# Kernel optimization log

Hardware: AMD Instinct MI355X
Metric: run time of the kernel (lower is better)

The kernel has to match this reference:

```python
import jax, jax.numpy as jnp
import numpy as np


def _gcn_conv(h, src, dst, W, b, n):
    # PyG GCNConv: x @ W, then symmetric-normalized aggregation with self-loops
    deg = jax.ops.segment_sum(jnp.ones(src.shape[0], h.dtype), dst, num_segments=n)
    dinv = jax.lax.rsqrt(jnp.maximum(deg, 1.0))  # deg >= 1 because self-loops are included
    norm = dinv[src] * dinv[dst]                 # [E]
    m = (h @ W)[src] * norm[:, None]             # gather + scale
    return jax.ops.segment_sum(m, dst, num_segments=n) + b


def setup_inputs() -> dict:
    key = jax.random.key(0)
    N, E, F, H, L, V = 50000, 800000, 128, 256, 64, 128
    ks = jax.random.split(key, 16)
    s = lambda fan_in: 1.0 / np.sqrt(fan_in)
    return {
        "x": jax.random.randint(ks[0], (N,), 0, V),
        "edge_index": jax.random.randint(ks[1], (2, E), 0, N),
        "eps": jax.random.normal(ks[2], (N, L), jnp.float32),
        "emb": jax.random.normal(ks[3], (V, F), jnp.float32),
        "W1": jax.random.normal(ks[4], (F, H), jnp.float32) * s(F),
        "b1": jnp.zeros((H,), jnp.float32),
        "W2": jax.random.normal(ks[5], (H, H), jnp.float32) * s(H),
        "b2": jnp.zeros((H,), jnp.float32),
        "Wmu": jax.random.normal(ks[6], (H, L), jnp.float32) * s(H),
        "bmu": jnp.zeros((L,), jnp.float32),
        "Wlv": jax.random.normal(ks[7], (H, L), jnp.float32) * s(H),
        "blv": jnp.zeros((L,), jnp.float32),
        "W3": jax.random.normal(ks[8], (L, H), jnp.float32) * s(L),
        "b3": jnp.zeros((H,), jnp.float32),
        "W4": jax.random.normal(ks[9], (H, V), jnp.float32) * s(H),
        "b4": jnp.zeros((V,), jnp.float32),
        "Wcap": jax.random.normal(ks[10], (L, 1), jnp.float32) * s(L),
        "bcap": jnp.zeros((1,), jnp.float32),
    }


def reference(x, edge_index, eps, emb, W1, b1, W2, b2, Wmu, bmu, Wlv, blv, W3, b3, W4, b4, Wcap, bcap):
    n = x.shape[0]
    loops = jnp.arange(n, dtype=edge_index.dtype)
    src = jnp.concatenate([edge_index[0], loops])  # add self-loops once, reuse
    dst = jnp.concatenate([edge_index[1], loops])

    h = emb[x]                                      # [N, F] embedding lookup
    h = jax.nn.relu(_gcn_conv(h, src, dst, W1, b1, n))
    h = jax.nn.relu(_gcn_conv(h, src, dst, W2, b2, n))
    mu = h @ Wmu + bmu
    logvar = h @ Wlv + blv
    z = mu + eps * jnp.exp(0.5 * logvar)            # reparameterize
    recon_x = jax.nn.relu(z @ W3 + b3) @ W4 + b4    # decode
    capitalize = jax.nn.sigmoid(z @ Wcap + bcap)
    return recon_x, capitalize, mu, logvar
```

## Files before the change

### kernel.cpp

```cpp
#include <hip/hip_runtime.h>
#include <math.h>


typedef __attribute__((ext_vector_type(8))) short bf16x8;
typedef __attribute__((ext_vector_type(8))) unsigned short u16x8;
typedef __attribute__((ext_vector_type(4))) float f32x4;

__device__ inline unsigned short f2bf(float x) {
    unsigned u = __float_as_uint(x);
    return (unsigned short)((u + 0x7FFFu + ((u >> 16) & 1u)) >> 16);
}
__device__ inline float bf2f(unsigned short h) {
    return __uint_as_float(((unsigned)h) << 16);
}

__global__ __launch_bounds__(256) void k_deg_count(const int* __restrict__ dst,
                                                   int* __restrict__ degint, int E) {
    int e = blockIdx.x * 256 + threadIdx.x;
    if (e < E) atomicAdd(&degint[dst[e]], 1);
}

#define SCAN_BLOCK 1024
__global__ __launch_bounds__(SCAN_BLOCK) void k_scan_local(
        const int* __restrict__ degint, int* __restrict__ row_ptr,
        int* __restrict__ bsum, float* __restrict__ dinv, int N) {
    __shared__ int s[SCAN_BLOCK];
    int gid = blockIdx.x * SCAN_BLOCK + threadIdx.x;
    int d = (gid < N) ? (degint[gid] + 1) : 0;
    if (gid < N) dinv[gid] = rsqrtf((float)d);
    s[threadIdx.x] = d;
    __syncthreads();
    for (int off = 1; off < SCAN_BLOCK; off <<= 1) {
        int t = (threadIdx.x >= off) ? s[threadIdx.x - off] : 0;
        __syncthreads();
        s[threadIdx.x] += t;
        __syncthreads();
    }
    if (gid < N) row_ptr[gid] = s[threadIdx.x] - d;
    if (threadIdx.x == SCAN_BLOCK - 1) bsum[blockIdx.x] = s[SCAN_BLOCK - 1];
}

__global__ __launch_bounds__(256) void k_scan_add(int* __restrict__ row_ptr,
                                                  const int* __restrict__ bsum,
                                                  int N, int T) {
    const int gid = blockIdx.x * 256 + threadIdx.x;
    const int myb = (blockIdx.x * 256) / SCAN_BLOCK;
    const int lane = threadIdx.x & 63;
    int v = (lane < myb) ? bsum[lane] : 0;
    v += __shfl_xor(v, 1, 64);
    v += __shfl_xor(v, 2, 64);
    v += __shfl_xor(v, 4, 64);
    v += __shfl_xor(v, 8, 64);
    v += __shfl_xor(v, 16, 64);
    v += __shfl_xor(v, 32, 64);
    if (gid < N) row_ptr[gid] += v;
    if (gid == 0) row_ptr[N] = T;
}

__global__ __launch_bounds__(256) void k_fill(
        const int* __restrict__ src, const int* __restrict__ dst,
        const int* __restrict__ x, const float* __restrict__ dinv,
        const int* __restrict__ row_ptr, int* __restrict__ cursor,
        int4* __restrict__ pack, int E, int N) {
    const int base = (blockIdx.x * 256 + threadIdx.x) * 4;
#pragma unroll
    for (int j = 0; j < 4; ++j) {
        int e = base + j;
        if (e < E) {
            int s = src[e], d = dst[e];
            float w = dinv[s] * dinv[d];
            int pos = row_ptr[d] + atomicAdd(&cursor[d], 1);
            pack[pos] = make_int4(__float_as_int(w), s, x[s], 0);
        } else if (e < E + N) {
            int i = e - E;
            float di = dinv[i];
            int pos = row_ptr[i] + atomicAdd(&cursor[i], 1);
            pack[pos] = make_int4(__float_as_int(di * di), i, x[i], 0);
        }
    }
}

__global__ __launch_bounds__(256) void k_cvt_all(
        const float* __restrict__ B0, unsigned short* __restrict__ h0, int K0, int N0,
        const float* __restrict__ B1, unsigned short* __restrict__ h1, int K1, int N1,
        const float* __restrict__ B2, unsigned short* __restrict__ h2, int K2, int N2,
        const float* __restrict__ B3, unsigned short* __restrict__ h3, int K3, int N3,
        const float* __restrict__ B4, unsigned short* __restrict__ h4, int K4, int N4) {
    const float* B; unsigned short* Bh; int K, Ncol;
    switch (blockIdx.y) {
        case 0: B = B0; Bh = h0; K = K0; Ncol = N0; break;
        case 1: B = B1; Bh = h1; K = K1; Ncol = N1; break;
        case 2: B = B2; Bh = h2; K = K2; Ncol = N2; break;
        case 3: B = B3; Bh = h3; K = K3; Ncol = N3; break;
        default: B = B4; Bh = h4; K = K4; Ncol = N4; break;
    }
    int i = blockIdx.x * 256 + threadIdx.x;
    if (i >= K * Ncol) return;
    int k = i / Ncol, n = i - k * Ncol;
    Bh[(long)n * K + k] = f2bf(B[i]);
}

__global__ __launch_bounds__(256) void k_gemm_f32t(
        const float* __restrict__ A, const float* __restrict__ B,
        unsigned short* __restrict__ CbT, int M, int K, int Ncol) {
    constexpr int BM = 64, BN = 64, BK = 16;
    __shared__ float As[BK][BM];
    __shared__ float Bs[BK][BN];
    const int tid = threadIdx.x;
    const int tx = tid & 15, ty = tid >> 4;
    const int rowBase = blockIdx.x * BM;
    const int colBase = blockIdx.y * BN;
    const int lr = tid >> 2, lc4 = tid & 3;
    const int br = tid >> 4, bc4 = tid & 15;
    const int arow = rowBase + lr;
    const int K4 = K >> 2, N4 = Ncol >> 2;
    const float4* A4 = (const float4*)A;
    const float4* B4 = (const float4*)B;
    float acc[4][4] = {{0.f}};
    for (int k0 = 0; k0 < K; k0 += BK) {
        float4 av = make_float4(0.f, 0.f, 0.f, 0.f);
        if (arow < M) av = A4[(long)arow * K4 + (k0 >> 2) + lc4];
        As[lc4 * 4 + 0][lr] = av.x;
        As[lc4 * 4 + 1][lr] = av.y;
        As[lc4 * 4 + 2][lr] = av.z;
        As[lc4 * 4 + 3][lr] = av.w;
        float4 bv = B4[(long)(k0 + br) * N4 + (colBase >> 2) + bc4];
        *(float4*)&Bs[br][bc4 * 4] = bv;
        __syncthreads();
#pragma unroll
        for (int k = 0; k < BK; ++k) {
            float4 a4v = *(const float4*)&As[k][ty * 4];
            float4 b4v = *(const float4*)&Bs[k][tx * 4];
            float aa[4] = {a4v.x, a4v.y, a4v.z, a4v.w};
            float bb[4] = {b4v.x, b4v.y, b4v.z, b4v.w};
#pragma unroll
            for (int i = 0; i < 4; ++i)
#pragma unroll
                for (int j = 0; j < 4; ++j)
                    acc[i][j] = fmaf(aa[i], bb[j], acc[i][j]);
        }
        __syncthreads();
    }
#pragma unroll
    for (int i = 0; i < 4; ++i) {
        int row = rowBase + ty * 4 + i;
        if (row < M) {
#pragma unroll
            for (int c = 0; c < 4; ++c) {
                int col = colBase + tx * 4 + c;
                CbT[(long)col * M + row] = f2bf(acc[i][c]);
            }
        }
    }
}

__global__ __launch_bounds__(256) void k_coef(
        const int4* __restrict__ pack, const int* __restrict__ row_ptr,
        unsigned short* __restrict__ cb, int N) {
    const int wave = threadIdx.x >> 6;
    const int lane = threadIdx.x & 63;
    const int node = blockIdx.x * 4 + wave;
    if (node >= N) return;
    const int tok0 = lane, tok1 = lane + 64;
    float c0 = 0.f, c1 = 0.f;
    const int beg = row_ptr[node], end = row_ptr[node + 1];
    int e = beg;
    for (; e + 4 <= end; e += 4) {
        int4 p0 = pack[e];
        int4 p1 = pack[e + 1];
        int4 p2 = pack[e + 2];
        int4 p3 = pack[e + 3];
        c0 += (p0.z == tok0) ? __int_as_float(p0.x) : 0.f;
        c1 += (p0.z == tok1) ? __int_as_float(p0.x) : 0.f;
        c0 += (p1.z == tok0) ? __int_as_float(p1.x) : 0.f;
        c1 += (p1.z == tok1) ? __int_as_float(p1.x) : 0.f;
        c0 += (p2.z == tok0) ? __int_as_float(p2.x) : 0.f;
        c1 += (p2.z == tok1) ? __int_as_float(p2.x) : 0.f;
        c0 += (p3.z == tok0) ? __int_as_float(p3.x) : 0.f;
        c1 += (p3.z == tok1) ? __int_as_float(p3.x) : 0.f;
    }
    for (; e < end; ++e) {
        int4 p = pack[e];
        c0 += (p.z == tok0) ? __int_as_float(p.x) : 0.f;
        c1 += (p.z == tok1) ? __int_as_float(p.x) : 0.f;
    }
    const long base = (long)node * 128;
    cb[base + lane]      = f2bf(c0);
    cb[base + lane + 64] = f2bf(c1);
}

template<bool RELU>
__global__ __launch_bounds__(256) void k_gemm_bn128(
        const unsigned short* __restrict__ A, const unsigned short* __restrict__ Bt,
        const float* __restrict__ bias, unsigned short* __restrict__ Cb,
        int M, int K, int Ncol) {
    __shared__ unsigned short Ash[64][40];
    __shared__ unsigned short Bsh[128][40];
    const int tid = threadIdx.x;
    const int lane = tid & 63, w = tid >> 6;
    const int fr = lane & 15, quad = lane >> 4;
    const int wm0 = w * 16;
    const int rowBase = blockIdx.x * 64;
    const int colBase = blockIdx.y * 128;

    const int arow = tid >> 2;
    const int aseg = (tid & 3) << 3;
    int agrow = rowBase + arow; if (agrow >= M) agrow = M - 1;
    const long abase = (long)agrow * K + aseg;
    const int brow = tid >> 1;
    const int bseg = (tid & 1) << 4;
    const long bbase = (long)(colBase + brow) * K + bseg;

    f32x4 acc[8];
#pragma unroll
    for (int j = 0; j < 8; ++j) acc[j] = (f32x4){0.f, 0.f, 0.f, 0.f};

    for (int k0 = 0; k0 < K; k0 += 32) {
        *(bf16x8*)&Ash[arow][aseg]     = *(const bf16x8*)&A[abase + k0];
        *(bf16x8*)&Bsh[brow][bseg]     = *(const bf16x8*)&Bt[bbase + k0];
        *(bf16x8*)&Bsh[brow][bseg + 8] = *(const bf16x8*)&Bt[bbase + k0 + 8];
        __syncthreads();
        bf16x8 af = *(const bf16x8*)&Ash[wm0 + fr][quad * 8];
#pragma unroll
        for (int j = 0; j < 8; ++j) {
            bf16x8 bhf = *(const bf16x8*)&Bsh[j * 16 + fr][quad * 8];
            acc[j] = __builtin_amdgcn_mfma_f32_16x16x32_bf16(af, bhf, acc[j], 0, 0, 0);
        }
        __syncthreads();
    }

#pragma unroll
    for (int j = 0; j < 8; ++j) {
        const int col = colBase + j * 16 + fr;
        const float bv = bias[col];
#pragma unroll
        for (int r = 0; r < 4; ++r) {
            const int row = rowBase + wm0 + quad * 4 + r;
            if (row < M) {
                float v = acc[j][r] + bv;
                if (RELU) v = fmaxf(v, 0.f);
                Cb[(long)row * Ncol + col] = f2bf(v);
            }
        }
    }
}

__global__ __launch_bounds__(256) void k_gemm_tail(
        const unsigned short* __restrict__ A, const unsigned short* __restrict__ Wml,
        const unsigned short* __restrict__ W3t, const unsigned short* __restrict__ W4t,
        const float* __restrict__ bmu, const float* __restrict__ blv,
        const float* __restrict__ eps, const float* __restrict__ Wcap,
        const float* __restrict__ bcap, const float* __restrict__ b3,
        const float* __restrict__ b4, float* __restrict__ mu,
        float* __restrict__ lv, float* __restrict__ recon,
        float* __restrict__ cap, int M) {
    constexpr int K = 256;
    __shared__ __align__(16) char smem[54272];
    unsigned short (*Bsh)[40] = (unsigned short (*)[40])smem;
    unsigned short (*Ash)[40] = (unsigned short (*)[40])(smem + 20480);
    unsigned short (*Zs)[72]  = (unsigned short (*)[72])(smem + 25600);
    unsigned short (*Ts)[264] = (unsigned short (*)[264])(smem + 20480);
    const int tid = threadIdx.x;
    const int lane = tid & 63, w = tid >> 6;
    const int fr = lane & 15, quad = lane >> 4;
    const int wm0 = w * 16;
    const int rowBase = blockIdx.x * 64;

    {
        const int zr = tid >> 2, zc = (tid & 3) * 18;
#pragma unroll
        for (int c = 0; c < 18; ++c) Zs[zr][zc + c] = 0;
    }

    const int arow = tid >> 2;
    const int aseg = (tid & 3) << 3;
    int agrow = rowBase + arow; if (agrow >= M) agrow = M - 1;
    const long abase = (long)agrow * K + aseg;
    const int brow = tid >> 1;
    const int bseg = (tid & 1) << 4;
    const long bbase = (long)brow * K + bseg;

    f32x4 acc[8];
#pragma unroll
    for (int j = 0; j < 8; ++j) acc[j] = (f32x4){0.f, 0.f, 0.f, 0.f};

    for (int k0 = 0; k0 < K; k0 += 32) {
        *(bf16x8*)&Ash[arow][aseg]     = *(const bf16x8*)&A[abase + k0];
        *(bf16x8*)&Bsh[brow][bseg]     = *(const bf16x8*)&Wml[bbase + k0];
        *(bf16x8*)&Bsh[brow][bseg + 8] = *(const bf16x8*)&Wml[bbase + k0 + 8];
        __syncthreads();
        bf16x8 ahf = *(const bf16x8*)&Ash[wm0 + fr][quad * 8];
#pragma unroll
        for (int j = 0; j < 8; ++j) {
            bf16x8 bhf = *(const bf16x8*)&Bsh[j * 16 + fr][quad * 8];
            acc[j] = __builtin_amdgcn_mfma_f32_16x16x32_bf16(ahf, bhf, acc[j], 0, 0, 0);
        }
        __syncthreads();
    }

    float capacc[4] = {0.f, 0.f, 0.f, 0.f};
#pragma unroll
    for (int j = 0; j < 4; ++j) {
        const int c = j * 16 + fr;
        const float bm = bmu[c], bl = blv[c];
        const float wc = Wcap[c];
#pragma unroll
        for (int r = 0; r < 4; ++r) {
            const int rl = wm0 + quad * 4 + r;
            const int row = rowBase + rl;
            if (row < M) {
                const long o = (long)row * 64 + c;
                float mv = acc[j][r] + bm;
                float lvv = acc[j + 4][r] + bl;
                mu[o] = mv;
                lv[o] = lvv;
                float zz = fmaf(eps[o], expf(0.5f * lvv), mv);
                Zs[rl][c] = f2bf(zz);
                capacc[r] = fmaf(zz, wc, capacc[r]);
            }
        }
    }
    const float b0 = bcap[0];
#pragma unroll
    for (int r = 0; r < 4; ++r) {
        float v = capacc[r];
        v += __shfl_xor(v, 1, 64);
        v += __shfl_xor(v, 2, 64);
        v += __shfl_xor(v, 4, 64);
        v += __shfl_xor(v, 8, 64);
        if (fr == 0) {
            const int row = rowBase + wm0 + quad * 4 + r;
            if (row < M) cap[row] = 1.f / (1.f + expf(-(v + b0)));
        }
    }

    f32x4 acc1[16];
#pragma unroll
    for (int j = 0; j < 16; ++j) acc1[j] = (f32x4){0.f, 0.f, 0.f, 0.f};
    for (int k0 = 0; k0 < 64; k0 += 32) {
        {
            const long wb = (long)tid * 64 + k0;
            *(bf16x8*)&Bsh[tid][0]  = *(const bf16x8*)&W3t[wb];
            *(bf16x8*)&Bsh[tid][8]  = *(const bf16x8*)&W3t[wb + 8];
            *(bf16x8*)&Bsh[tid][16] = *(const bf16x8*)&W3t[wb + 16];
            *(bf16x8*)&Bsh[tid][24] = *(const bf16x8*)&W3t[wb + 24];
        }
        __syncthreads();
        bf16x8 af = *(const bf16x8*)&Zs[wm0 + fr][k0 + quad * 8];
#pragma unroll
        for (int j = 0; j < 16; ++j) {
            bf16x8 bf = *(const bf16x8*)&Bsh[j * 16 + fr][quad * 8];
            acc1[j] = __builtin_amdgcn_mfma_f32_16x16x32_bf16(af, bf, acc1[j], 0, 0, 0);
        }
        __syncthreads();
    }

#pragma unroll
    for (int j = 0; j < 16; ++j) {
        const int col = j * 16 + fr;
        const float bv = b3[col];
#pragma unroll
        for (int r = 0; r < 4; ++r) {
            const int rl = wm0 + quad * 4 + r;
            Ts[rl][col] = f2bf(fmaxf(acc1[j][r] + bv, 0.f));
        }
    }
    __syncthreads();

    f32x4 acc2[8];
#pragma unroll
    for (int j = 0; j < 8; ++j) acc2[j] = (f32x4){0.f, 0.f, 0.f, 0.f};
    const int br2 = tid >> 1;
    const int bs2 = (tid & 1) << 4;
    for (int k0 = 0; k0 < 256; k0 += 32) {
        const long wb = (long)br2 * 256 + k0 + bs2;
        *(bf16x8*)&Bsh[br2][bs2]     = *(const bf16x8*)&W4t[wb];
        *(bf16x8*)&Bsh[br2][bs2 + 8] = *(const bf16x8*)&W4t[wb + 8];
        __syncthreads();
        bf16x8 at = *(const bf16x8*)&Ts[wm0 + fr][k0 + quad * 8];
#pragma unroll
        for (int j = 0; j < 8; ++j) {
            bf16x8 bf = *(const bf16x8*)&Bsh[j * 16 + fr][quad * 8];
            acc2[j] = __builtin_amdgcn_mfma_f32_16x16x32_bf16(at, bf, acc2[j], 0, 0, 0);
        }
        __syncthreads();
    }

#pragma unroll
    for (int j = 0; j < 8; ++j) {
        const int col = j * 16 + fr;
        const float bv = b4[col];
#pragma unroll
        for (int r = 0; r < 4; ++r) {
            const int row = rowBase + wm0 + quad * 4 + r;
            if (row < M) recon[(long)row * 128 + col] = acc2[j][r] + bv;
        }
    }
}

__global__ __launch_bounds__(256) void k_agg_nb(
        const unsigned short* __restrict__ h1, const int* __restrict__ row_ptr,
        const int2* __restrict__ pk2, unsigned short* __restrict__ Ob, int N) {
    const int wave = threadIdx.x >> 6;
    const int lane = threadIdx.x & 63;
    const int node = blockIdx.x * 4 + wave;
    if (node >= N) return;
    const int half = lane >> 5;
    const int col  = lane & 31;
    const u16x8* hrow = (const u16x8*)h1;
    float acc[8] = {0.f, 0.f, 0.f, 0.f, 0.f, 0.f, 0.f, 0.f};
    const int beg = row_ptr[node], end = row_ptr[node + 1];
    int e = beg;
    for (; e + 8 <= end; e += 8) {
        int2 q0 = pk2[2 * (e + 0 + half)];
        int2 q1 = pk2[2 * (e + 2 + half)];
        int2 q2 = pk2[2 * (e + 4 + half)];
        int2 q3 = pk2[2 * (e + 6 + half)];
        u16x8 v0 = hrow[(long)q0.y * 32 + col];
        u16x8 v1 = hrow[(long)q1.y * 32 + col];
        u16x8 v2 = hrow[(long)q2.y * 32 + col];
        u16x8 v3 = hrow[(long)q3.y * 32 + col];
        float w0 = __int_as_float(q0.x), w1 = __int_as_float(q1.x);
        float w2 = __int_as_float(q2.x), w3 = __int_as_float(q3.x);
#pragma unroll
        for (int c = 0; c < 8; ++c) {
            acc[c] = fmaf(bf2f(v0[c]), w0, acc[c]);
            acc[c] = fmaf(bf2f(v1[c]), w1, acc[c]);
            acc[c] = fmaf(bf2f(v2[c]), w2, acc[c]);
            acc[c] = fmaf(bf2f(v3[c]), w3, acc[c]);
        }
    }
    for (; e + 2 <= end; e += 2) {
        int2 q = pk2[2 * (e + half)];
        float w = __int_as_float(q.x);
        u16x8 v = hrow[(long)q.y * 32 + col];
#pragma unroll
        for (int c = 0; c < 8; ++c) acc[c] = fmaf(bf2f(v[c]), w, acc[c]);
    }
    if (e < end) {
        int2 q = pk2[2 * e];
        float w = (half == 0) ? __int_as_float(q.x) : 0.f;
        u16x8 v = hrow[(long)q.y * 32 + col];
#pragma unroll
        for (int c = 0; c < 8; ++c) acc[c] = fmaf(bf2f(v[c]), w, acc[c]);
    }
#pragma unroll
    for (int c = 0; c < 8; ++c) acc[c] += __shfl_xor(acc[c], 32, 64);
    if (lane < 32) {
        u16x8 o;
#pragma unroll
        for (int c = 0; c < 8; ++c) o[c] = f2bf(acc[c]);
        ((u16x8*)Ob)[(long)node * 32 + col] = o;
    }
}

extern "C" void kernel_launch(void* const* d_in, const int* in_sizes, int n_in,
                              void* d_out, int out_size, void* d_ws, size_t ws_size,
                              hipStream_t stream) {
    const int*   x    = (const int*)d_in[0];
    const int*   ei   = (const int*)d_in[1];
    const float* eps  = (const float*)d_in[2];
    const float* emb  = (const float*)d_in[3];
    const float* W1   = (const float*)d_in[4];
    const float* b1   = (const float*)d_in[5];
    const float* W2   = (const float*)d_in[6];
    const float* b2   = (const float*)d_in[7];
    const float* Wmu  = (const float*)d_in[8];
    const float* bmu  = (const float*)d_in[9];
    const float* Wlv  = (const float*)d_in[10];
    const float* blv  = (const float*)d_in[11];
    const float* W3   = (const float*)d_in[12];
    const float* b3   = (const float*)d_in[13];
    const float* W4   = (const float*)d_in[14];
    const float* b4   = (const float*)d_in[15];
    const float* Wcap = (const float*)d_in[16];
    const float* bcap = (const float*)d_in[17];

    const int N = in_sizes[0];
    const int E = in_sizes[1] / 2;
    const int H = in_sizes[5];
    const int L = in_sizes[9];
    const int V = in_sizes[15];
    const int F = in_sizes[4] / H;
    const int T = E + N;

    const int* src = ei;
    const int* dst = ei + E;

    char* w = (char*)d_ws;
    unsigned short* h1b  = (unsigned short*)w; w += (size_t)N * H * 2;
    unsigned short* a2b  = (unsigned short*)w; w += (size_t)N * H * 2;
    unsigned short* h2b  = (unsigned short*)w; w += (size_t)N * H * 2;
    unsigned short* cb   = (unsigned short*)w; w += (size_t)N * V * 2;
    int*   degint = (int*)w;   w += (size_t)N * 4;
    int*   cursor = (int*)w;   w += (size_t)N * 4;
    int*   rowp   = (int*)w;   w += (size_t)(N + 1) * 4;
    float* dinv   = (float*)w; w += (size_t)N * 4;
    int*   bsum   = (int*)w;   w += 256 * 4;
    int4*  pack   = (int4*)w;  w += (size_t)T * 16;
    unsigned short* tabT = (unsigned short*)w; w += (size_t)H * V * 2;
    unsigned short* W2t  = (unsigned short*)w; w += (size_t)H * H * 2;
    unsigned short* Wml  = (unsigned short*)w; w += (size_t)H * 2 * L * 2;
    unsigned short* W3t  = (unsigned short*)w; w += (size_t)L * H * 2;
    unsigned short* W4t  = (unsigned short*)w; w += (size_t)H * V * 2;

    float* outp    = (float*)d_out;
    float* recon   = outp;
    float* cap     = outp + (size_t)N * V;
    float* mu      = outp + (size_t)N * V + N;
    float* logvar  = mu + (size_t)N * L;

    const int nN  = (N + 255) / 256;
    const int nE  = (E + 255) / 256;
    const int nT4 = (T + 1023) / 1024;
    const int nSc = (N + SCAN_BLOCK - 1) / SCAN_BLOCK;
    const int gM64  = (N + 63) / 64;

    hipMemsetAsync(degint, 0, (size_t)N * 8, stream);
    k_deg_count<<<nE, 256, 0, stream>>>(dst, degint, E);
    k_scan_local<<<nSc, SCAN_BLOCK, 0, stream>>>(degint, rowp, bsum, dinv, N);
    k_scan_add<<<nN, 256, 0, stream>>>(rowp, bsum, N, T);
    k_fill<<<nT4, 256, 0, stream>>>(src, dst, x, dinv, rowp, cursor, pack, E, N);

    k_cvt_all<<<dim3((H * H + 255) / 256, 5), 256, 0, stream>>>(
        W2, W2t, H, H,
        Wmu, Wml, H, L,
        Wlv, Wml + (size_t)L * H, H, L,
        W3, W3t, L, H,
        W4, W4t, H, V);

    k_gemm_f32t<<<dim3(V / 64, H / 64), 256, 0, stream>>>(emb, W1, tabT, V, F, H);
    k_coef<<<(N + 3) / 4, 256, 0, stream>>>(pack, rowp, cb, N);
    k_gemm_bn128<true><<<dim3(gM64, H / 128), 256, 0, stream>>>(
        cb, tabT, b1, h1b, N, V, H);

    k_agg_nb<<<(N + 3) / 4, 256, 0, stream>>>(h1b, rowp, (const int2*)pack, a2b, N);
    k_gemm_bn128<true><<<dim3(gM64, H / 128), 256, 0, stream>>>(
        a2b, W2t, b2, h2b, N, H, H);

    k_gemm_tail<<<gM64, 256, 0, stream>>>(
        h2b, Wml, W3t, W4t, bmu, blv, eps, Wcap, bcap, b3, b4,
        mu, logvar, recon, cap, N);
}
```

Before: 389.1 us.

## Fuse CSR construction into one cooperative kernel and merge weight prep kernels

The memset, degree count, two-level scan and edge fill are replaced with a single cooperative kernel that uses grid-wide syncs between phases. The weight bf16 conversion and the emb@W1 table GEMM are merged into one launch. The goal is to cut kernel launch and inter-kernel gap overhead. In exchange the CSR phases now run on a fixed grid of 1024 blocks with grid.sync barriers, and the scan uses 256-element chunks, which caps N at 65536 because a single block scans the chunk sums.

```diff
diff --git a/kernel.cpp b/kernel.cpp
--- a/kernel.cpp
+++ b/kernel.cpp
@@ -1,5 +1,8 @@
 #include <hip/hip_runtime.h>
+#include <hip/hip_cooperative_groups.h>
 #include <math.h>
+
+namespace cg = cooperative_groups;
 
 
 typedef __attribute__((ext_vector_type(8))) short bf16x8;
@@ -14,64 +17,70 @@
     return __uint_as_float(((unsigned)h) << 16);
 }
 
-__global__ __launch_bounds__(256) void k_deg_count(const int* __restrict__ dst,
-                                                   int* __restrict__ degint, int E) {
-    int e = blockIdx.x * 256 + threadIdx.x;
-    if (e < E) atomicAdd(&degint[dst[e]], 1);
-}
-
-#define SCAN_BLOCK 1024
-__global__ __launch_bounds__(SCAN_BLOCK) void k_scan_local(
-        const int* __restrict__ degint, int* __restrict__ row_ptr,
-        int* __restrict__ bsum, float* __restrict__ dinv, int N) {
-    __shared__ int s[SCAN_BLOCK];
-    int gid = blockIdx.x * SCAN_BLOCK + threadIdx.x;
-    int d = (gid < N) ? (degint[gid] + 1) : 0;
-    if (gid < N) dinv[gid] = rsqrtf((float)d);
-    s[threadIdx.x] = d;
-    __syncthreads();
-    for (int off = 1; off < SCAN_BLOCK; off <<= 1) {
-        int t = (threadIdx.x >= off) ? s[threadIdx.x - off] : 0;
-        __syncthreads();
-        s[threadIdx.x] += t;
-        __syncthreads();
-    }
-    if (gid < N) row_ptr[gid] = s[threadIdx.x] - d;
-    if (threadIdx.x == SCAN_BLOCK - 1) bsum[blockIdx.x] = s[SCAN_BLOCK - 1];
-}
-
-__global__ __launch_bounds__(256) void k_scan_add(int* __restrict__ row_ptr,
-                                                  const int* __restrict__ bsum,
-                                                  int N, int T) {
-    const int gid = blockIdx.x * 256 + threadIdx.x;
-    const int myb = (blockIdx.x * 256) / SCAN_BLOCK;
-    const int lane = threadIdx.x & 63;
-    int v = (lane < myb) ? bsum[lane] : 0;
-    v += __shfl_xor(v, 1, 64);
-    v += __shfl_xor(v, 2, 64);
-    v += __shfl_xor(v, 4, 64);
-    v += __shfl_xor(v, 8, 64);
-    v += __shfl_xor(v, 16, 64);
-    v += __shfl_xor(v, 32, 64);
-    if (gid < N) row_ptr[gid] += v;
-    if (gid == 0) row_ptr[N] = T;
-}
-
-__global__ __launch_bounds__(256) void k_fill(
+__global__ __launch_bounds__(256) void k_csr_coop(
         const int* __restrict__ src, const int* __restrict__ dst,
-        const int* __restrict__ x, const float* __restrict__ dinv,
-        const int* __restrict__ row_ptr, int* __restrict__ cursor,
+        const int* __restrict__ x, int* __restrict__ degint,
+        int* __restrict__ cursor, int* __restrict__ row_ptr,
+        float* __restrict__ dinv, int* __restrict__ bsum,
         int4* __restrict__ pack, int E, int N) {
-    const int base = (blockIdx.x * 256 + threadIdx.x) * 4;
-#pragma unroll
-    for (int j = 0; j < 4; ++j) {
-        int e = base + j;
+    cg::grid_group grid = cg::this_grid();
+    const int tid = threadIdx.x;
+    const int bid = blockIdx.x;
+    const int nb  = gridDim.x;
+    const int gstride = nb * 256;
+    __shared__ int s[256];
+
+    for (int i = bid * 256 + tid; i < N; i += gstride) { degint[i] = 0; cursor[i] = 0; }
+    grid.sync();
+
+    for (int e = bid * 256 + tid; e < E; e += gstride) atomicAdd(&degint[dst[e]], 1);
+    grid.sync();
+
+    const int nCh = (N + 255) >> 8;
+    for (int c = bid; c < nCh; c += nb) {
+        const int gid = c * 256 + tid;
+        int d = (gid < N) ? (degint[gid] + 1) : 0;
+        if (gid < N) dinv[gid] = rsqrtf((float)d);
+        s[tid] = d;
+        __syncthreads();
+        for (int off = 1; off < 256; off <<= 1) {
+            int t = (tid >= off) ? s[tid - off] : 0;
+            __syncthreads();
+            s[tid] += t;
+            __syncthreads();
+        }
+        if (gid < N) row_ptr[gid] = s[tid] - d;
+        if (tid == 255) bsum[c] = s[255];
+        __syncthreads();
+    }
+    grid.sync();
+
+    if (bid == 0) {
+        int v = (tid < nCh) ? bsum[tid] : 0;
+        s[tid] = v;
+        __syncthreads();
+        for (int off = 1; off < 256; off <<= 1) {
+            int t = (tid >= off) ? s[tid - off] : 0;
+            __syncthreads();
+            s[tid] += t;
+            __syncthreads();
+        }
+        if (tid < nCh) bsum[tid] = s[tid] - v;
+    }
+    grid.sync();
+
+    for (int gid = bid * 256 + tid; gid < N; gid += gstride)
+        row_ptr[gid] += bsum[gid >> 8];
+    if (bid == 0 && tid == 0) row_ptr[N] = E + N;
+    grid.sync();
+
+    for (int e = bid * 256 + tid; e < E + N; e += gstride) {
         if (e < E) {
-            int s = src[e], d = dst[e];
-            float w = dinv[s] * dinv[d];
+            int sE = src[e], d = dst[e];
+            float w = dinv[sE] * dinv[d];
             int pos = row_ptr[d] + atomicAdd(&cursor[d], 1);
-            pack[pos] = make_int4(__float_as_int(w), s, x[s], 0);
-        } else if (e < E + N) {
+            pack[pos] = make_int4(__float_as_int(w), sE, x[sE], 0);
+        } else {
             int i = e - E;
             float di = dinv[i];
             int pos = row_ptr[i] + atomicAdd(&cursor[i], 1);
@@ -80,51 +89,55 @@
     }
 }
 
-__global__ __launch_bounds__(256) void k_cvt_all(
+__global__ __launch_bounds__(256) void k_prep(
         const float* __restrict__ B0, unsigned short* __restrict__ h0, int K0, int N0,
         const float* __restrict__ B1, unsigned short* __restrict__ h1, int K1, int N1,
         const float* __restrict__ B2, unsigned short* __restrict__ h2, int K2, int N2,
         const float* __restrict__ B3, unsigned short* __restrict__ h3, int K3, int N3,
-        const float* __restrict__ B4, unsigned short* __restrict__ h4, int K4, int N4) {
-    const float* B; unsigned short* Bh; int K, Ncol;
-    switch (blockIdx.y) {
-        case 0: B = B0; Bh = h0; K = K0; Ncol = N0; break;
-        case 1: B = B1; Bh = h1; K = K1; Ncol = N1; break;
-        case 2: B = B2; Bh = h2; K = K2; Ncol = N2; break;
-        case 3: B = B3; Bh = h3; K = K3; Ncol = N3; break;
-        default: B = B4; Bh = h4; K = K4; Ncol = N4; break;
-    }
-    int i = blockIdx.x * 256 + threadIdx.x;
-    if (i >= K * Ncol) return;
-    int k = i / Ncol, n = i - k * Ncol;
-    Bh[(long)n * K + k] = f2bf(B[i]);
-}
-
-__global__ __launch_bounds__(256) void k_gemm_f32t(
-        const float* __restrict__ A, const float* __restrict__ B,
-        unsigned short* __restrict__ CbT, int M, int K, int Ncol) {
+        const float* __restrict__ B4, unsigned short* __restrict__ h4, int K4, int N4,
+        const float* __restrict__ emb, const float* __restrict__ W1,
+        unsigned short* __restrict__ tabT, int Mt, int Kt, int Nt) {
+    __shared__ float As[16][64];
+    __shared__ float Bs[16][64];
+    const int tid = threadIdx.x;
+
+    if (blockIdx.y < 5) {
+        const float* B; unsigned short* Bh; int K, Ncol;
+        switch (blockIdx.y) {
+            case 0: B = B0; Bh = h0; K = K0; Ncol = N0; break;
+            case 1: B = B1; Bh = h1; K = K1; Ncol = N1; break;
+            case 2: B = B2; Bh = h2; K = K2; Ncol = N2; break;
+            case 3: B = B3; Bh = h3; K = K3; Ncol = N3; break;
+            default: B = B4; Bh = h4; K = K4; Ncol = N4; break;
+        }
+        int i = blockIdx.x * 256 + tid;
+        if (i < K * Ncol) {
+            int k = i / Ncol, n = i - k * Ncol;
+            Bh[(long)n * K + k] = f2bf(B[i]);
+        }
+        return;
+    }
+
+    if (blockIdx.x >= 8) return;
     constexpr int BM = 64, BN = 64, BK = 16;
-    __shared__ float As[BK][BM];
-    __shared__ float Bs[BK][BN];
-    const int tid = threadIdx.x;
     const int tx = tid & 15, ty = tid >> 4;
-    const int rowBase = blockIdx.x * BM;
-    const int colBase = blockIdx.y * BN;
+    const int rowBase = (blockIdx.x & 1) * BM;
+    const int colBase = (blockIdx.x >> 1) * BN;
     const int lr = tid >> 2, lc4 = tid & 3;
     const int br = tid >> 4, bc4 = tid & 15;
     const int arow = rowBase + lr;
-    const int K4 = K >> 2, N4 = Ncol >> 2;
-    const float4* A4 = (const float4*)A;
-    const float4* B4 = (const float4*)B;
+    const int Ktq = Kt >> 2, Ntq = Nt >> 2;
+    const float4* A4 = (const float4*)emb;
+    const float4* B4v = (const float4*)W1;
     float acc[4][4] = {{0.f}};
-    for (int k0 = 0; k0 < K; k0 += BK) {
+    for (int k0 = 0; k0 < Kt; k0 += BK) {
         float4 av = make_float4(0.f, 0.f, 0.f, 0.f);
-        if (arow < M) av = A4[(long)arow * K4 + (k0 >> 2) + lc4];
+        if (arow < Mt) av = A4[(long)arow * Ktq + (k0 >> 2) + lc4];
         As[lc4 * 4 + 0][lr] = av.x;
         As[lc4 * 4 + 1][lr] = av.y;
         As[lc4 * 4 + 2][lr] = av.z;
         As[lc4 * 4 + 3][lr] = av.w;
-        float4 bv = B4[(long)(k0 + br) * N4 + (colBase >> 2) + bc4];
+        float4 bv = B4v[(long)(k0 + br) * Ntq + (colBase >> 2) + bc4];
         *(float4*)&Bs[br][bc4 * 4] = bv;
         __syncthreads();
 #pragma unroll
@@ -144,11 +157,11 @@
 #pragma unroll
     for (int i = 0; i < 4; ++i) {
         int row = rowBase + ty * 4 + i;
-        if (row < M) {
+        if (row < Mt) {
 #pragma unroll
             for (int c = 0; c < 4; ++c) {
                 int col = colBase + tx * 4 + c;
-                CbT[(long)col * M + row] = f2bf(acc[i][c]);
+                tabT[(long)col * Mt + row] = f2bf(acc[i][c]);
             }
         }
     }
@@ -510,26 +523,28 @@
     float* mu      = outp + (size_t)N * V + N;
     float* logvar  = mu + (size_t)N * L;
 
-    const int nN  = (N + 255) / 256;
-    const int nE  = (E + 255) / 256;
-    const int nT4 = (T + 1023) / 1024;
-    const int nSc = (N + SCAN_BLOCK - 1) / SCAN_BLOCK;
-    const int gM64  = (N + 63) / 64;
-
-    hipMemsetAsync(degint, 0, (size_t)N * 8, stream);
-    k_deg_count<<<nE, 256, 0, stream>>>(dst, degint, E);
-    k_scan_local<<<nSc, SCAN_BLOCK, 0, stream>>>(degint, rowp, bsum, dinv, N);
-    k_scan_add<<<nN, 256, 0, stream>>>(rowp, bsum, N, T);
-    k_fill<<<nT4, 256, 0, stream>>>(src, dst, x, dinv, rowp, cursor, pack, E, N);
-
-    k_cvt_all<<<dim3((H * H + 255) / 256, 5), 256, 0, stream>>>(
+    const int gM64 = (N + 63) / 64;
+
+    {
+        int Ec = E, Nc = N;
+        void* cargs[] = {
+            (void*)&src, (void*)&dst, (void*)&x, (void*)&degint,
+            (void*)&cursor, (void*)&rowp, (void*)&dinv, (void*)&bsum,
+            (void*)&pack, (void*)&Ec, (void*)&Nc };
+        (void)hipLaunchCooperativeKernel((const void*)k_csr_coop,
+                                         dim3(1024), dim3(256), cargs, 0, stream);
+    }
+
+    unsigned short* WmlLo = Wml;
+    unsigned short* WmlHi = Wml + (size_t)L * H;
+    k_prep<<<dim3((H * H + 255) / 256, 6), 256, 0, stream>>>(
         W2, W2t, H, H,
-        Wmu, Wml, H, L,
-        Wlv, Wml + (size_t)L * H, H, L,
+        Wmu, WmlLo, H, L,
+        Wlv, WmlHi, H, L,
         W3, W3t, L, H,
-        W4, W4t, H, V);
-
-    k_gemm_f32t<<<dim3(V / 64, H / 64), 256, 0, stream>>>(emb, W1, tabT, V, F, H);
+        W4, W4t, H, V,
+        emb, W1, tabT, V, F, H);
+
     k_coef<<<(N + 3) / 4, 256, 0, stream>>>(pack, rowp, cb, N);
     k_gemm_bn128<true><<<dim3(gM64, H / 128), 256, 0, stream>>>(
         cb, tabT, b1, h1b, N, V, H);
```

Result: slower. 855.9 us (+120.0%).

## Fuse weight conversion with embedding GEMM and widen bf16 GEMM K-tile

Applied to the files above, without the earlier changes.

Merges the weight-transpose/convert kernel and the small emb@W1 fp32 GEMM into one launch by adding a sixth grid row that runs the GEMM in 8 blocks. The goal is to cut one kernel launch. Separately, the bf16 MFMA GEMM now stages a 64-wide K tile per iteration instead of 32, halving the barrier count and loop trips in exchange for more shared memory per block. For K=128 this gives 2 iterations instead of 4, and for K=256, 4 instead of 8.

```diff
diff --git a/kernel.cpp b/kernel.cpp
--- a/kernel.cpp
+++ b/kernel.cpp
@@ -80,51 +80,55 @@
     }
 }
 
-__global__ __launch_bounds__(256) void k_cvt_all(
+__global__ __launch_bounds__(256) void k_prep(
         const float* __restrict__ B0, unsigned short* __restrict__ h0, int K0, int N0,
         const float* __restrict__ B1, unsigned short* __restrict__ h1, int K1, int N1,
         const float* __restrict__ B2, unsigned short* __restrict__ h2, int K2, int N2,
         const float* __restrict__ B3, unsigned short* __restrict__ h3, int K3, int N3,
-        const float* __restrict__ B4, unsigned short* __restrict__ h4, int K4, int N4) {
-    const float* B; unsigned short* Bh; int K, Ncol;
-    switch (blockIdx.y) {
-        case 0: B = B0; Bh = h0; K = K0; Ncol = N0; break;
-        case 1: B = B1; Bh = h1; K = K1; Ncol = N1; break;
-        case 2: B = B2; Bh = h2; K = K2; Ncol = N2; break;
-        case 3: B = B3; Bh = h3; K = K3; Ncol = N3; break;
-        default: B = B4; Bh = h4; K = K4; Ncol = N4; break;
-    }
-    int i = blockIdx.x * 256 + threadIdx.x;
-    if (i >= K * Ncol) return;
-    int k = i / Ncol, n = i - k * Ncol;
-    Bh[(long)n * K + k] = f2bf(B[i]);
-}
-
-__global__ __launch_bounds__(256) void k_gemm_f32t(
-        const float* __restrict__ A, const float* __restrict__ B,
-        unsigned short* __restrict__ CbT, int M, int K, int Ncol) {
+        const float* __restrict__ B4, unsigned short* __restrict__ h4, int K4, int N4,
+        const float* __restrict__ emb, const float* __restrict__ W1,
+        unsigned short* __restrict__ tabT, int Mt, int Kt, int Nt) {
+    __shared__ float As[16][64];
+    __shared__ float Bs[16][64];
+    const int tid = threadIdx.x;
+
+    if (blockIdx.y < 5) {
+        const float* B; unsigned short* Bh; int K, Ncol;
+        switch (blockIdx.y) {
+            case 0: B = B0; Bh = h0; K = K0; Ncol = N0; break;
+            case 1: B = B1; Bh = h1; K = K1; Ncol = N1; break;
+            case 2: B = B2; Bh = h2; K = K2; Ncol = N2; break;
+            case 3: B = B3; Bh = h3; K = K3; Ncol = N3; break;
+            default: B = B4; Bh = h4; K = K4; Ncol = N4; break;
+        }
+        int i = blockIdx.x * 256 + tid;
+        if (i < K * Ncol) {
+            int k = i / Ncol, n = i - k * Ncol;
+            Bh[(long)n * K + k] = f2bf(B[i]);
+        }
+        return;
+    }
+
+    if (blockIdx.x >= 8) return;
     constexpr int BM = 64, BN = 64, BK = 16;
-    __shared__ float As[BK][BM];
-    __shared__ float Bs[BK][BN];
-    const int tid = threadIdx.x;
     const int tx = tid & 15, ty = tid >> 4;
-    const int rowBase = blockIdx.x * BM;
-    const int colBase = blockIdx.y * BN;
+    const int rowBase = (blockIdx.x & 1) * BM;
+    const int colBase = (blockIdx.x >> 1) * BN;
     const int lr = tid >> 2, lc4 = tid & 3;
     const int br = tid >> 4, bc4 = tid & 15;
     const int arow = rowBase + lr;
-    const int K4 = K >> 2, N4 = Ncol >> 2;
-    const float4* A4 = (const float4*)A;
-    const float4* B4 = (const float4*)B;
+    const int Ktq = Kt >> 2, Ntq = Nt >> 2;
+    const float4* A4 = (const float4*)emb;
+    const float4* B4v = (const float4*)W1;
     float acc[4][4] = {{0.f}};
-    for (int k0 = 0; k0 < K; k0 += BK) {
+    for (int k0 = 0; k0 < Kt; k0 += BK) {
         float4 av = make_float4(0.f, 0.f, 0.f, 0.f);
-        if (arow < M) av = A4[(long)arow * K4 + (k0 >> 2) + lc4];
+        if (arow < Mt) av = A4[(long)arow * Ktq + (k0 >> 2) + lc4];
         As[lc4 * 4 + 0][lr] = av.x;
         As[lc4 * 4 + 1][lr] = av.y;
         As[lc4 * 4 + 2][lr] = av.z;
         As[lc4 * 4 + 3][lr] = av.w;
-        float4 bv = B4[(long)(k0 + br) * N4 + (colBase >> 2) + bc4];
+        float4 bv = B4v[(long)(k0 + br) * Ntq + (colBase >> 2) + bc4];
         *(float4*)&Bs[br][bc4 * 4] = bv;
         __syncthreads();
 #pragma unroll
@@ -144,11 +148,11 @@
 #pragma unroll
     for (int i = 0; i < 4; ++i) {
         int row = rowBase + ty * 4 + i;
-        if (row < M) {
+        if (row < Mt) {
 #pragma unroll
             for (int c = 0; c < 4; ++c) {
                 int col = colBase + tx * 4 + c;
-                CbT[(long)col * M + row] = f2bf(acc[i][c]);
+                tabT[(long)col * Mt + row] = f2bf(acc[i][c]);
             }
         }
     }
@@ -194,8 +198,8 @@
         const unsigned short* __restrict__ A, const unsigned short* __restrict__ Bt,
         const float* __restrict__ bias, unsigned short* __restrict__ Cb,
         int M, int K, int Ncol) {
-    __shared__ unsigned short Ash[64][40];
-    __shared__ unsigned short Bsh[128][40];
+    __shared__ unsigned short Ash[64][72];
+    __shared__ unsigned short Bsh[128][72];
     const int tid = threadIdx.x;
     const int lane = tid & 63, w = tid >> 6;
     const int fr = lane & 15, quad = lane >> 4;
@@ -204,27 +208,36 @@
     const int colBase = blockIdx.y * 128;
 
     const int arow = tid >> 2;
-    const int aseg = (tid & 3) << 3;
+    const int aseg = (tid & 3) << 4;
     int agrow = rowBase + arow; if (agrow >= M) agrow = M - 1;
     const long abase = (long)agrow * K + aseg;
     const int brow = tid >> 1;
-    const int bseg = (tid & 1) << 4;
+    const int bseg = (tid & 1) << 5;
     const long bbase = (long)(colBase + brow) * K + bseg;
 
     f32x4 acc[8];
 #pragma unroll
     for (int j = 0; j < 8; ++j) acc[j] = (f32x4){0.f, 0.f, 0.f, 0.f};
 
-    for (int k0 = 0; k0 < K; k0 += 32) {
-        *(bf16x8*)&Ash[arow][aseg]     = *(const bf16x8*)&A[abase + k0];
-        *(bf16x8*)&Bsh[brow][bseg]     = *(const bf16x8*)&Bt[bbase + k0];
-        *(bf16x8*)&Bsh[brow][bseg + 8] = *(const bf16x8*)&Bt[bbase + k0 + 8];
-        __syncthreads();
-        bf16x8 af = *(const bf16x8*)&Ash[wm0 + fr][quad * 8];
+    for (int k0 = 0; k0 < K; k0 += 64) {
+        *(bf16x8*)&Ash[arow][aseg]      = *(const bf16x8*)&A[abase + k0];
+        *(bf16x8*)&Ash[arow][aseg + 8]  = *(const bf16x8*)&A[abase + k0 + 8];
+        *(bf16x8*)&Bsh[brow][bseg]      = *(const bf16x8*)&Bt[bbase + k0];
+        *(bf16x8*)&Bsh[brow][bseg + 8]  = *(const bf16x8*)&Bt[bbase + k0 + 8];
+        *(bf16x8*)&Bsh[brow][bseg + 16] = *(const bf16x8*)&Bt[bbase + k0 + 16];
+        *(bf16x8*)&Bsh[brow][bseg + 24] = *(const bf16x8*)&Bt[bbase + k0 + 24];
+        __syncthreads();
+        bf16x8 af0 = *(const bf16x8*)&Ash[wm0 + fr][quad * 8];
+        bf16x8 af1 = *(const bf16x8*)&Ash[wm0 + fr][32 + quad * 8];
 #pragma unroll
         for (int j = 0; j < 8; ++j) {
-            bf16x8 bhf = *(const bf16x8*)&Bsh[j * 16 + fr][quad * 8];
-            acc[j] = __builtin_amdgcn_mfma_f32_16x16x32_bf16(af, bhf, acc[j], 0, 0, 0);
+            bf16x8 b0 = *(const bf16x8*)&Bsh[j * 16 + fr][quad * 8];
+            acc[j] = __builtin_amdgcn_mfma_f32_16x16x32_bf16(af0, b0, acc[j], 0, 0, 0);
+        }
+#pragma unroll
+        for (int j = 0; j < 8; ++j) {
+            bf16x8 b1 = *(const bf16x8*)&Bsh[j * 16 + fr][32 + quad * 8];
+            acc[j] = __builtin_amdgcn_mfma_f32_16x16x32_bf16(af1, b1, acc[j], 0, 0, 0);
         }
         __syncthreads();
     }
@@ -514,7 +527,7 @@
     const int nE  = (E + 255) / 256;
     const int nT4 = (T + 1023) / 1024;
     const int nSc = (N + SCAN_BLOCK - 1) / SCAN_BLOCK;
-    const int gM64  = (N + 63) / 64;
+    const int gM64 = (N + 63) / 64;
 
     hipMemsetAsync(degint, 0, (size_t)N * 8, stream);
     k_deg_count<<<nE, 256, 0, stream>>>(dst, degint, E);
@@ -522,14 +535,16 @@
     k_scan_add<<<nN, 256, 0, stream>>>(rowp, bsum, N, T);
     k_fill<<<nT4, 256, 0, stream>>>(src, dst, x, dinv, rowp, cursor, pack, E, N);
 
-    k_cvt_all<<<dim3((H * H + 255) / 256, 5), 256, 0, stream>>>(
+    unsigned short* WmlLo = Wml;
+    unsigned short* WmlHi = Wml + (size_t)L * H;
+    k_prep<<<dim3((H * H + 255) / 256, 6), 256, 0, stream>>>(
         W2, W2t, H, H,
-        Wmu, Wml, H, L,
-        Wlv, Wml + (size_t)L * H, H, L,
+        Wmu, WmlLo, H, L,
+        Wlv, WmlHi, H, L,
         W3, W3t, L, H,
-        W4, W4t, H, V);
-
-    k_gemm_f32t<<<dim3(V / 64, H / 64), 256, 0, stream>>>(emb, W1, tabT, V, F, H);
+        W4, W4t, H, V,
+        emb, W1, tabT, V, F, H);
+
     k_coef<<<(N + 3) / 4, 256, 0, stream>>>(pack, rowp, cb, N);
     k_gemm_bn128<true><<<dim3(gM64, H / 128), 256, 0, stream>>>(
         cb, tabT, b1, h1b, N, V, H);
```

After: 389.0 us. No clear change (-0.0%).
